# Kernel tuning notes

Hardware: AMD Instinct MI355X
Metric: run time of the kernel (lower is better)

## Reference

```python
import jax, jax.numpy as jnp
import numpy as np
import math

D_MODEL = 1024
N_HEADS = 16
D_HEAD = D_MODEL // N_HEADS
WINDOW = 256
SCALE = 1.0 / math.sqrt(D_HEAD)


def setup_inputs() -> dict:
    key = jax.random.key(0)
    kx, kqkv, kout = jax.random.split(key, 3)
    x = jax.random.normal(kx, (2, 2048, D_MODEL), dtype=jnp.float32)
    # xavier_uniform for nn.Linear weights (shape [out, in] in torch; store as [in, out] for x @ W)
    lim_qkv = math.sqrt(6.0 / (D_MODEL + 3 * D_MODEL))
    W_qkv = jax.random.uniform(kqkv, (D_MODEL, 3 * D_MODEL), dtype=jnp.float32, minval=-lim_qkv, maxval=lim_qkv)
    lim_out = math.sqrt(6.0 / (D_MODEL + D_MODEL))
    W_out = jax.random.uniform(kout, (D_MODEL, D_MODEL), dtype=jnp.float32, minval=-lim_out, maxval=lim_out)
    return {"x": x, "W_qkv": W_qkv, "W_out": W_out}


def _window_mask(seq_len: int) -> jnp.ndarray:
    # causal + sliding window: position i attends to j with i-WINDOW < j <= i
    i = jnp.arange(seq_len)[:, None]
    j = jnp.arange(seq_len)[None, :]
    allowed = (j <= i) & (j > i - WINDOW)
    return jnp.where(allowed, 0.0, -jnp.inf).astype(jnp.float32)


def reference(x, W_qkv, W_out):
    B, S, _ = x.shape
    qkv = x @ W_qkv                                   # [B, S, 3*D]
    qkv = qkv.reshape(B, S, 3, N_HEADS, D_HEAD)
    qkv = jnp.transpose(qkv, (2, 0, 3, 1, 4))         # [3, B, H, S, Dh]
    q, k, v = qkv[0], qkv[1], qkv[2]
    scores = jnp.einsum('bhsd,bhtd->bhst', q, k) * SCALE
    scores = scores + _window_mask(S)[None, None]
    weights = jax.nn.softmax(scores, axis=-1)
    out = jnp.einsum('bhst,bhtd->bhsd', weights, v)   # [B, H, S, Dh]
    out = jnp.transpose(out, (0, 2, 1, 3)).reshape(B, S, D_MODEL)
    return out @ W_out
```

## Files before the change

### kernel.cpp

```cpp
#include <hip/hip_runtime.h>

typedef unsigned short u16;
typedef unsigned int u32;

#define D_MODEL 1024
#define N_HEADS 16
#define D_HEAD 64
#define WIN 256
#define SEQ 2048
#define BATCH 2
#define NROWS (BATCH*SEQ)

typedef short frag_ab __attribute__((ext_vector_type(8)));
typedef float frag_cd __attribute__((ext_vector_type(4)));
typedef float f32x16 __attribute__((ext_vector_type(16)));
typedef u16 u16x8 __attribute__((ext_vector_type(8)));

__device__ __forceinline__ u16 f2bf(float f) {
    union { float f; u32 u; } x; x.f = f;
    u32 r = x.u + 0x7fffu + ((x.u >> 16) & 1u);
    return (u16)(r >> 16);
}

__device__ __forceinline__ void load_lds16(const void* g, void* l) {
    __builtin_amdgcn_global_load_lds(
        (const __attribute__((address_space(1))) void*)g,
        (__attribute__((address_space(3))) void*)l, 16, 0, 0);
}

__device__ __forceinline__ void transpose_tile(const float* __restrict__ W, u16* __restrict__ WT,
                                               int K, int N, int n0, int k0,
                                               int scale_rows, float scale, float (*tile)[33]) {
    int x = threadIdx.x & 31, y = threadIdx.x >> 5;
#pragma unroll
    for (int r = 0; r < 4; r++)
        tile[y + 8 * r][x] = W[(size_t)(k0 + y + 8 * r) * N + n0 + x];
    __syncthreads();
#pragma unroll
    for (int r = 0; r < 4; r++) {
        int nrow = n0 + y + 8 * r;
        float v = tile[x][y + 8 * r];
        if (nrow < scale_rows) v *= scale;
        WT[(size_t)nrow * K + k0 + x] = f2bf(v);
    }
}

__global__ __launch_bounds__(256) void prep_kernel(const float* __restrict__ x,
                                                   const float* __restrict__ W_qkv,
                                                   u16* __restrict__ xb,
                                                   u16* __restrict__ wqkvT,
                                                   float qscale) {
    __shared__ float tile[32][33];
    const int bid = blockIdx.x;
    if (bid < 4096) {
        int idx = bid * 256 + threadIdx.x;
        float4 v = ((const float4*)x)[idx];
        ushort4 o;
        o.x = f2bf(v.x); o.y = f2bf(v.y); o.z = f2bf(v.z); o.w = f2bf(v.w);
        ((ushort4*)xb)[idx] = o;
    } else {
        int t = bid - 4096;
        transpose_tile(W_qkv, wqkvT, D_MODEL, 3 * D_MODEL, (t % 96) * 32, (t / 96) * 32,
                       D_MODEL, qscale, tile);
    }
}

__global__ __launch_bounds__(512, 2) void gemm1_qkv(const u16* __restrict__ A,
                                                    const u16* __restrict__ BT,
                                                    u16* __restrict__ C) {
    constexpr int K = 1024, NLD = 3072, NT = K >> 6;
    __shared__ union SM {
        struct { u16 As[2][256 * 64]; u16 Bs[2][192 * 64]; } s;
        u16 cs[256 * 200];
    } sm;
    const int tid = threadIdx.x;
    const int xcd = blockIdx.x & 7, sblk = blockIdx.x >> 3;
    const int m0 = (sblk & 15) * 256;
    const int n0 = (xcd * 2 + (sblk >> 4)) * 192;
    const int wave = tid >> 6, lane = tid & 63;
    const int wm = (wave >> 1) * 64, wn = (wave & 1) * 96;
    const int l32 = lane & 31, kh = lane >> 5;

    const int r0 = tid >> 3;
    const int w  = (tid & 7) ^ (r0 & 7);
    const u16* aP = A  + (size_t)(m0 + r0) * K + w * 8;
    const u16* bP = BT + (size_t)(n0 + r0) * K + w * 8;

    f32x16 acc[2][3] = {};

#define STAGE(tile_, buf_) do {                                                   \
        const int k0_ = (tile_) * 64;                                             \
        _Pragma("unroll")                                                         \
        for (int u = 0; u < 4; ++u)                                               \
            load_lds16(aP + (size_t)(64 * u) * K + k0_,                           \
                       &sm.s.As[buf_][(tid + 512 * u) * 8]);                      \
        _Pragma("unroll")                                                         \
        for (int u = 0; u < 3; ++u)                                               \
            load_lds16(bP + (size_t)(64 * u) * K + k0_,                           \
                       &sm.s.Bs[buf_][(tid + 512 * u) * 8]);                      \
    } while (0)

    STAGE(0, 0);
    STAGE(1, 1);

    int cur = 0;
    for (int t = 0; t < NT; ++t) {
        if (t + 1 < NT) asm volatile("s_waitcnt vmcnt(7)" ::: "memory");
        else            asm volatile("s_waitcnt vmcnt(0)" ::: "memory");
        asm volatile("s_barrier" ::: "memory");

        const u16* As = sm.s.As[cur];
        const u16* Bs = sm.s.Bs[cur];
#pragma unroll
        for (int ph = 0; ph < 2; ++ph) {
            frag_ab af[2][2], bf[2][3];
#pragma unroll
            for (int kx = 0; kx < 2; ++kx) {
                const int kk = ph * 2 + kx;
                const int csel = ((kk * 2 + kh) ^ (l32 & 7)) * 8;
#pragma unroll
                for (int mt = 0; mt < 2; ++mt)
                    af[kx][mt] = *(const frag_ab*)&As[(wm + mt * 32 + l32) * 64 + csel];
#pragma unroll
                for (int nt = 0; nt < 3; ++nt)
                    bf[kx][nt] = *(const frag_ab*)&Bs[(wn + nt * 32 + l32) * 64 + csel];
            }
            asm volatile("s_barrier" ::: "memory");
            __builtin_amdgcn_s_setprio(1);
#pragma unroll
            for (int kx = 0; kx < 2; ++kx)
#pragma unroll
                for (int mt = 0; mt < 2; ++mt)
#pragma unroll
                    for (int nt = 0; nt < 3; ++nt)
                        acc[mt][nt] = __builtin_amdgcn_mfma_f32_32x32x16_bf16(
                            af[kx][mt], bf[kx][nt], acc[mt][nt], 0, 0, 0);
            __builtin_amdgcn_s_setprio(0);
            asm volatile("s_barrier" ::: "memory");
        }
        if (t + 2 < NT) STAGE(t + 2, cur);
        cur ^= 1;
    }
#undef STAGE

#pragma unroll
    for (int mt = 0; mt < 2; ++mt)
#pragma unroll
        for (int nt = 0; nt < 3; ++nt) {
            const int col = wn + nt * 32 + l32;
#pragma unroll
            for (int reg = 0; reg < 16; ++reg) {
                const int row = wm + mt * 32 + (reg & 3) + 8 * (reg >> 2) + 4 * kh;
                sm.cs[row * 200 + col] = f2bf(acc[mt][nt][reg]);
            }
        }
    asm volatile("s_barrier" ::: "memory");
#pragma unroll
    for (int i = 0; i < 12; ++i) {
        const int idx = tid + 512 * i;
        const int row = idx / 24, c8 = idx % 24;
        u16x8 vv = *(const u16x8*)&sm.cs[row * 200 + c8 * 8];
        *(u16x8*)(C + (size_t)(m0 + row) * NLD + n0 + c8 * 8) = vv;
    }
}

template <bool BF16_OUT, int BM, int MB, int NPER>
__global__ __launch_bounds__(256, 4) void gemm_bk64(const u16* __restrict__ A,
                                                    const u16* __restrict__ BT,
                                                    void* __restrict__ C,
                                                    int M, int N, int K) {
    constexpr int MT = BM / 64;
    __shared__ union SMem {
        struct { u16 As[BM * 64]; u16 Bs[128 * 64]; } s;
        u16 cs[BF16_OUT ? BM * 136 : 1];
    } sm;
    const int tid = threadIdx.x;
    const int xcd = blockIdx.x & 7, sblk = blockIdx.x >> 3;
    const int m0 = (sblk % MB) * BM;
    const int n0 = (xcd * NPER + sblk / MB) * 128;
    const int wave = tid >> 6, lane = tid & 63;
    const int wm = (wave >> 1) * (BM / 2), wn = (wave & 1) * 64;
    const int l32 = lane & 31, kh = lane >> 5;

    f32x16 acc[MT][2] = {};

    const int r0 = tid >> 3;
    const int w  = (tid & 7) ^ (r0 & 7);
    const u16* aP = A  + (size_t)(m0 + r0) * K + w * 8;
    const u16* bP = BT + (size_t)(n0 + r0) * K + w * 8;

    for (int k0 = 0; k0 < K; k0 += 64) {
        __syncthreads();
#pragma unroll
        for (int u = 0; u < BM / 32; u++)
            load_lds16(aP + (size_t)(32 * u) * K + k0, &sm.s.As[(tid + 256 * u) * 8]);
#pragma unroll
        for (int u = 0; u < 4; u++)
            load_lds16(bP + (size_t)(32 * u) * K + k0, &sm.s.Bs[(tid + 256 * u) * 8]);
        __syncthreads();

#pragma unroll
        for (int kk = 0; kk < 4; kk++) {
            const int csel = ((kk * 2 + kh) ^ (l32 & 7)) * 8;
            frag_ab af[MT], bf[2];
#pragma unroll
            for (int t = 0; t < MT; t++)
                af[t] = *(const frag_ab*)&sm.s.As[(wm + t * 32 + l32) * 64 + csel];
#pragma unroll
            for (int t = 0; t < 2; t++)
                bf[t] = *(const frag_ab*)&sm.s.Bs[(wn + t * 32 + l32) * 64 + csel];
#pragma unroll
            for (int mt = 0; mt < MT; mt++)
#pragma unroll
                for (int nt = 0; nt < 2; nt++)
                    acc[mt][nt] = __builtin_amdgcn_mfma_f32_32x32x16_bf16(af[mt], bf[nt], acc[mt][nt], 0, 0, 0);
        }
    }

    if constexpr (BF16_OUT) {
        __syncthreads();
#pragma unroll
        for (int mt = 0; mt < MT; mt++)
#pragma unroll
            for (int nt = 0; nt < 2; nt++) {
                int col = wn + nt * 32 + l32;
#pragma unroll
                for (int reg = 0; reg < 16; reg++) {
                    int row = wm + mt * 32 + (reg & 3) + 8 * (reg >> 2) + 4 * kh;
                    sm.cs[row * 136 + col] = f2bf(acc[mt][nt][reg]);
                }
            }
        __syncthreads();
        const int cc = tid & 15, rb = tid >> 4;
#pragma unroll
        for (int i = 0; i < BM / 16; i++) {
            int row = rb + 16 * i;
            u16x8 vv = *(const u16x8*)&sm.cs[row * 136 + cc * 8];
            *(u16x8*)((u16*)C + (size_t)(m0 + row) * N + n0 + cc * 8) = vv;
        }
    } else {
#pragma unroll
        for (int mt = 0; mt < MT; mt++)
#pragma unroll
            for (int nt = 0; nt < 2; nt++) {
                int col = n0 + wn + nt * 32 + l32;
#pragma unroll
                for (int reg = 0; reg < 16; reg++) {
                    int row = m0 + wm + mt * 32 + (reg & 3) + 8 * (reg >> 2) + 4 * kh;
                    ((float*)C)[(size_t)row * N + col] = acc[mt][nt][reg];
                }
            }
    }
}

__global__ __launch_bounds__(256) void attn_kernel(const u16* __restrict__ qkv, u16* __restrict__ out,
                                                   const float* __restrict__ W_out,
                                                   u16* __restrict__ woutT) {
    __shared__ u16 Ks[2][64 * 64];
    __shared__ u16 Vt[64 * 72];
    __shared__ u16 ps[4][16 * 72];

    if (blockIdx.x >= 1024) {
        int t = blockIdx.x - 1024;
        transpose_tile(W_out, woutT, D_MODEL, D_MODEL, (t & 31) * 32, (t >> 5) * 32,
                       0, 1.0f, (float(*)[33])&Ks[0][0]);
        return;
    }

    const int tid = threadIdx.x;
    const int wave = tid >> 6, lane = tid & 63;
    const int quad = lane >> 4, c16 = lane & 15;

    const int bh = blockIdx.x & 31;
    const int qc = blockIdx.x >> 5;
    const int h  = bh & 15;
    const int b  = bh >> 4;
    const int q0 = qc * 64;
    const int qw0 = q0 + wave * 16;

    frag_ab qf[2];
    {
        const u16* qrow = qkv + (size_t)(b * SEQ + qw0 + c16) * 3072 + h * 64;
        qf[0] = *(const frag_ab*)(qrow + quad * 8);
        qf[1] = *(const frag_ab*)(qrow + 32 + quad * 8);
    }

    float m_r[4], l_r[4];
    frag_cd acc[4] = {};

    const int ntiles = qc < 4 ? qc + 1 : 5;

    const int krow = wave * 16 + (lane >> 3);
    const int kchunk = (lane & 7) ^ (lane >> 3);
    const int vj2 = (tid & 31) * 2, vd8 = tid >> 5;

    const u16* kbase = qkv + (size_t)(b * SEQ + krow) * 3072 + 1024 + h * 64 + kchunk * 8;
    const u16* vbase = qkv + (size_t)(b * SEQ + vj2) * 3072 + 2048 + h * 64 + vd8 * 8;

    u16x8 va, vb;
    {
        const u16* g = kbase + (size_t)q0 * 3072;
        load_lds16(g,            &Ks[0][krow * 64 + (lane & 7) * 8]);
        load_lds16(g + 8 * 3072, &Ks[0][(krow + 8) * 64 + (lane & 7) * 8]);
        const u16* gv = vbase + (size_t)q0 * 3072;
        va = *(const u16x8*)gv;
        vb = *(const u16x8*)(gv + 3072);
#pragma unroll
        for (int dd = 0; dd < 8; dd++)
            *(u32*)&Vt[(vd8 * 8 + dd) * 72 + vj2] = (u32)va[dd] | ((u32)vb[dd] << 16);
    }

    for (int t = 0; t < ntiles; t++) {
        const int cur = t & 1, nxt = cur ^ 1;
        const int j0 = q0 - 64 * t;
        __syncthreads();
        const bool pre = (t + 1 < ntiles);
        if (pre) {
            const u16* g = kbase + (size_t)(j0 - 64) * 3072;
            load_lds16(g,            &Ks[nxt][krow * 64 + (lane & 7) * 8]);
            load_lds16(g + 8 * 3072, &Ks[nxt][(krow + 8) * 64 + (lane & 7) * 8]);
            const u16* gv = vbase + (size_t)(j0 - 64) * 3072;
            va = *(const u16x8*)gv;
            vb = *(const u16x8*)(gv + 3072);
        }

        frag_cd s[4] = {};
#pragma unroll
        for (int kb = 0; kb < 4; kb++) {
            frag_ab kf0 = *(const frag_ab*)&Ks[cur][(kb * 16 + c16) * 64 + ((quad    ) ^ (c16 & 7)) * 8];
            frag_ab kf1 = *(const frag_ab*)&Ks[cur][(kb * 16 + c16) * 64 + ((4 + quad) ^ (c16 & 7)) * 8];
            s[kb] = __builtin_amdgcn_mfma_f32_16x16x32_bf16(qf[0], kf0, s[kb], 0, 0, 0);
            s[kb] = __builtin_amdgcn_mfma_f32_16x16x32_bf16(qf[1], kf1, s[kb], 0, 0, 0);
        }

        if (t == 0) {
#pragma unroll
            for (int reg = 0; reg < 4; reg++) {
                const int i = qw0 + quad * 4 + reg;
#pragma unroll
                for (int kb = 0; kb < 4; kb++)
                    if (q0 + kb * 16 + c16 > i) s[kb][reg] = -1e30f;
            }
        } else if (t == 4) {
#pragma unroll
            for (int reg = 0; reg < 4; reg++) {
                const int i = qw0 + quad * 4 + reg;
#pragma unroll
                for (int kb = 0; kb < 4; kb++)
                    if (j0 + kb * 16 + c16 + WIN <= i) s[kb][reg] = -1e30f;
            }
        }

        float mt_[4];
#pragma unroll
        for (int reg = 0; reg < 4; reg++)
            mt_[reg] = fmaxf(fmaxf(s[0][reg], s[1][reg]), fmaxf(s[2][reg], s[3][reg]));
#pragma unroll
        for (int off = 1; off < 16; off <<= 1)
#pragma unroll
            for (int reg = 0; reg < 4; reg++) mt_[reg] = fmaxf(mt_[reg], __shfl_xor(mt_[reg], off));

        float alpha[4];
        if (t == 0) {
#pragma unroll
            for (int reg = 0; reg < 4; reg++) m_r[reg] = mt_[reg];
        } else {
#pragma unroll
            for (int reg = 0; reg < 4; reg++) {
                float mn = fmaxf(m_r[reg], mt_[reg]);
                alpha[reg] = __builtin_amdgcn_exp2f(m_r[reg] - mn);
                m_r[reg] = mn;
            }
        }

        float rs[4] = {0.f, 0.f, 0.f, 0.f};
#pragma unroll
        for (int kb = 0; kb < 4; kb++)
#pragma unroll
            for (int reg = 0; reg < 4; reg++) {
                float p = __builtin_amdgcn_exp2f(s[kb][reg] - m_r[reg]);
                union { float f; u32 u; } pu; pu.f = p;
                ps[wave][(quad * 4 + reg) * 72 + kb * 16 + c16] = (u16)(pu.u >> 16);
                rs[reg] += p;
            }
#pragma unroll
        for (int off = 1; off < 16; off <<= 1)
#pragma unroll
            for (int reg = 0; reg < 4; reg++) rs[reg] += __shfl_xor(rs[reg], off);

        if (t == 0) {
#pragma unroll
            for (int reg = 0; reg < 4; reg++) l_r[reg] = rs[reg];
        } else {
#pragma unroll
            for (int reg = 0; reg < 4; reg++) l_r[reg] = l_r[reg] * alpha[reg] + rs[reg];
#pragma unroll
            for (int dblk = 0; dblk < 4; dblk++)
#pragma unroll
                for (int reg = 0; reg < 4; reg++) acc[dblk][reg] *= alpha[reg];
        }

#pragma unroll
        for (int js = 0; js < 2; js++) {
            frag_ab pf = *(const frag_ab*)&ps[wave][c16 * 72 + js * 32 + quad * 8];
#pragma unroll
            for (int dblk = 0; dblk < 4; dblk++) {
                frag_ab vf = *(const frag_ab*)&Vt[(dblk * 16 + c16) * 72 + js * 32 + quad * 8];
                acc[dblk] = __builtin_amdgcn_mfma_f32_16x16x32_bf16(pf, vf, acc[dblk], 0, 0, 0);
            }
        }

        if (pre) {
            __syncthreads();
#pragma unroll
            for (int dd = 0; dd < 8; dd++)
                *(u32*)&Vt[(vd8 * 8 + dd) * 72 + vj2] = (u32)va[dd] | ((u32)vb[dd] << 16);
        }
    }

    float inv[4];
#pragma unroll
    for (int reg = 0; reg < 4; reg++) inv[reg] = 1.f / l_r[reg];
#pragma unroll
    for (int dblk = 0; dblk < 4; dblk++)
#pragma unroll
        for (int reg = 0; reg < 4; reg++)
            out[(size_t)(b * SEQ + qw0 + quad * 4 + reg) * 1024 + h * 64 + dblk * 16 + c16] =
                f2bf(acc[dblk][reg] * inv[reg]);
}

extern "C" void kernel_launch(void* const* d_in, const int* in_sizes, int n_in,
                              void* d_out, int out_size, void* d_ws, size_t ws_size,
                              hipStream_t stream) {
    const float* x     = (const float*)d_in[0];
    const float* W_qkv = (const float*)d_in[1];
    const float* W_out = (const float*)d_in[2];
    float* out = (float*)d_out;

    char* ws = (char*)d_ws;
    u16* xb    = (u16*)(ws);
    u16* wqkvT = (u16*)(ws + 8388608);
    u16* woutT = (u16*)(ws + 14680064);
    u16* qkvb  = (u16*)(ws + 16777216);
    u16* attnb = (u16*)(ws + 41943040);

    const float QSCALE = 0.125f * 1.4426950408889634f;

    prep_kernel<<<7168, 256, 0, stream>>>(x, W_qkv, xb, wqkvT, QSCALE);
    gemm1_qkv<<<256, 512, 0, stream>>>(xb, wqkvT, qkvb);
    attn_kernel<<<2048, 256, 0, stream>>>(qkvb, attnb, W_out, woutT);
    gemm_bk64<false, 64, 64, 1><<<512, 256, 0, stream>>>(
        attnb, woutT, out, NROWS, D_MODEL, D_MODEL);
}
```

Measured before the change: 151.6 us.

## Replace output GEMM with double-buffered 128x128 tiled kernel; restructure QKV GEMM phases

Replaces the generic single-buffered output projection GEMM with a dedicated kernel that uses 128x128 tiles, double-buffered LDS staging with async loads, and phased fragment loads with priority hints. It now launches 256 blocks instead of 512, each doing more work. The QKV GEMM inner loop is also changed from two phases of two k-steps to four single k-step phases, which adds more barriers but keeps fewer fragments live. The intent is to overlap global loads with MFMA in the output GEMM and reduce per-tile overhead, at the cost of fewer blocks to fill the CUs.

```diff
diff --git a/kernel.cpp b/kernel.cpp
--- a/kernel.cpp
+++ b/kernel.cpp
@@ -112,29 +112,23 @@
         const u16* As = sm.s.As[cur];
         const u16* Bs = sm.s.Bs[cur];
 #pragma unroll
-        for (int ph = 0; ph < 2; ++ph) {
-            frag_ab af[2][2], bf[2][3];
-#pragma unroll
-            for (int kx = 0; kx < 2; ++kx) {
-                const int kk = ph * 2 + kx;
-                const int csel = ((kk * 2 + kh) ^ (l32 & 7)) * 8;
-#pragma unroll
-                for (int mt = 0; mt < 2; ++mt)
-                    af[kx][mt] = *(const frag_ab*)&As[(wm + mt * 32 + l32) * 64 + csel];
-#pragma unroll
-                for (int nt = 0; nt < 3; ++nt)
-                    bf[kx][nt] = *(const frag_ab*)&Bs[(wn + nt * 32 + l32) * 64 + csel];
-            }
+        for (int kk = 0; kk < 4; ++kk) {
+            const int csel = ((kk * 2 + kh) ^ (l32 & 7)) * 8;
+            frag_ab af[2], bf[3];
+#pragma unroll
+            for (int mt = 0; mt < 2; ++mt)
+                af[mt] = *(const frag_ab*)&As[(wm + mt * 32 + l32) * 64 + csel];
+#pragma unroll
+            for (int nt = 0; nt < 3; ++nt)
+                bf[nt] = *(const frag_ab*)&Bs[(wn + nt * 32 + l32) * 64 + csel];
             asm volatile("s_barrier" ::: "memory");
             __builtin_amdgcn_s_setprio(1);
 #pragma unroll
-            for (int kx = 0; kx < 2; ++kx)
-#pragma unroll
-                for (int mt = 0; mt < 2; ++mt)
-#pragma unroll
-                    for (int nt = 0; nt < 3; ++nt)
-                        acc[mt][nt] = __builtin_amdgcn_mfma_f32_32x32x16_bf16(
-                            af[kx][mt], bf[kx][nt], acc[mt][nt], 0, 0, 0);
+            for (int mt = 0; mt < 2; ++mt)
+#pragma unroll
+                for (int nt = 0; nt < 3; ++nt)
+                    acc[mt][nt] = __builtin_amdgcn_mfma_f32_32x32x16_bf16(
+                        af[mt], bf[nt], acc[mt][nt], 0, 0, 0);
             __builtin_amdgcn_s_setprio(0);
             asm volatile("s_barrier" ::: "memory");
         }
@@ -164,93 +158,92 @@
     }
 }
 
-template <bool BF16_OUT, int BM, int MB, int NPER>
-__global__ __launch_bounds__(256, 4) void gemm_bk64(const u16* __restrict__ A,
-                                                    const u16* __restrict__ BT,
-                                                    void* __restrict__ C,
-                                                    int M, int N, int K) {
-    constexpr int MT = BM / 64;
-    __shared__ union SMem {
-        struct { u16 As[BM * 64]; u16 Bs[128 * 64]; } s;
-        u16 cs[BF16_OUT ? BM * 136 : 1];
-    } sm;
+__global__ __launch_bounds__(256) void gemm2_out(const u16* __restrict__ A,
+                                                 const u16* __restrict__ BT,
+                                                 float* __restrict__ C) {
+    constexpr int K = 1024, N = 1024, NT = K >> 6;
+    __shared__ struct { u16 As[2][128 * 64]; u16 Bs[2][128 * 64]; } sm;
     const int tid = threadIdx.x;
     const int xcd = blockIdx.x & 7, sblk = blockIdx.x >> 3;
-    const int m0 = (sblk % MB) * BM;
-    const int n0 = (xcd * NPER + sblk / MB) * 128;
+    const int m0 = sblk * 128;
+    const int n0 = xcd * 128;
     const int wave = tid >> 6, lane = tid & 63;
-    const int wm = (wave >> 1) * (BM / 2), wn = (wave & 1) * 64;
+    const int wm = (wave >> 1) * 64, wn = (wave & 1) * 64;
     const int l32 = lane & 31, kh = lane >> 5;
-
-    f32x16 acc[MT][2] = {};
 
     const int r0 = tid >> 3;
     const int w  = (tid & 7) ^ (r0 & 7);
     const u16* aP = A  + (size_t)(m0 + r0) * K + w * 8;
     const u16* bP = BT + (size_t)(n0 + r0) * K + w * 8;
 
-    for (int k0 = 0; k0 < K; k0 += 64) {
-        __syncthreads();
-#pragma unroll
-        for (int u = 0; u < BM / 32; u++)
-            load_lds16(aP + (size_t)(32 * u) * K + k0, &sm.s.As[(tid + 256 * u) * 8]);
-#pragma unroll
-        for (int u = 0; u < 4; u++)
-            load_lds16(bP + (size_t)(32 * u) * K + k0, &sm.s.Bs[(tid + 256 * u) * 8]);
-        __syncthreads();
-
-#pragma unroll
-        for (int kk = 0; kk < 4; kk++) {
-            const int csel = ((kk * 2 + kh) ^ (l32 & 7)) * 8;
-            frag_ab af[MT], bf[2];
-#pragma unroll
-            for (int t = 0; t < MT; t++)
-                af[t] = *(const frag_ab*)&sm.s.As[(wm + t * 32 + l32) * 64 + csel];
-#pragma unroll
-            for (int t = 0; t < 2; t++)
-                bf[t] = *(const frag_ab*)&sm.s.Bs[(wn + t * 32 + l32) * 64 + csel];
-#pragma unroll
-            for (int mt = 0; mt < MT; mt++)
-#pragma unroll
-                for (int nt = 0; nt < 2; nt++)
-                    acc[mt][nt] = __builtin_amdgcn_mfma_f32_32x32x16_bf16(af[mt], bf[nt], acc[mt][nt], 0, 0, 0);
-        }
-    }
-
-    if constexpr (BF16_OUT) {
-        __syncthreads();
-#pragma unroll
-        for (int mt = 0; mt < MT; mt++)
-#pragma unroll
-            for (int nt = 0; nt < 2; nt++) {
-                int col = wn + nt * 32 + l32;
-#pragma unroll
-                for (int reg = 0; reg < 16; reg++) {
-                    int row = wm + mt * 32 + (reg & 3) + 8 * (reg >> 2) + 4 * kh;
-                    sm.cs[row * 136 + col] = f2bf(acc[mt][nt][reg]);
-                }
-            }
-        __syncthreads();
-        const int cc = tid & 15, rb = tid >> 4;
-#pragma unroll
-        for (int i = 0; i < BM / 16; i++) {
-            int row = rb + 16 * i;
-            u16x8 vv = *(const u16x8*)&sm.cs[row * 136 + cc * 8];
-            *(u16x8*)((u16*)C + (size_t)(m0 + row) * N + n0 + cc * 8) = vv;
-        }
-    } else {
-#pragma unroll
-        for (int mt = 0; mt < MT; mt++)
-#pragma unroll
-            for (int nt = 0; nt < 2; nt++) {
-                int col = n0 + wn + nt * 32 + l32;
-#pragma unroll
-                for (int reg = 0; reg < 16; reg++) {
-                    int row = m0 + wm + mt * 32 + (reg & 3) + 8 * (reg >> 2) + 4 * kh;
-                    ((float*)C)[(size_t)row * N + col] = acc[mt][nt][reg];
-                }
-            }
-    }
+    f32x16 acc[2][2] = {};
+
+#define STAGE2(tile_, buf_) do {                                                  \
+        const int k0_ = (tile_) * 64;                                             \
+        _Pragma("unroll")                                                         \
+        for (int u = 0; u < 4; ++u)                                               \
+            load_lds16(aP + (size_t)(32 * u) * K + k0_,                           \
+                       &sm.As[buf_][(tid + 256 * u) * 8]);                        \
+        _Pragma("unroll")                                                         \
+        for (int u = 0; u < 4; ++u)                                               \
+            load_lds16(bP + (size_t)(32 * u) * K + k0_,                           \
+                       &sm.Bs[buf_][(tid + 256 * u) * 8]);                        \
+    } while (0)
+
+    STAGE2(0, 0);
+    STAGE2(1, 1);
+
+    int cur = 0;
+    for (int t = 0; t < NT; ++t) {
+        if (t + 1 < NT) asm volatile("s_waitcnt vmcnt(8)" ::: "memory");
+        else            asm volatile("s_waitcnt vmcnt(0)" ::: "memory");
+        asm volatile("s_barrier" ::: "memory");
+
+        const u16* As = sm.As[cur];
+        const u16* Bs = sm.Bs[cur];
+#pragma unroll
+        for (int ph = 0; ph < 2; ++ph) {
+            frag_ab af[2][2], bf[2][2];
+#pragma unroll
+            for (int kx = 0; kx < 2; ++kx) {
+                const int kk = ph * 2 + kx;
+                const int csel = ((kk * 2 + kh) ^ (l32 & 7)) * 8;
+#pragma unroll
+                for (int mt = 0; mt < 2; ++mt)
+                    af[kx][mt] = *(const frag_ab*)&As[(wm + mt * 32 + l32) * 64 + csel];
+#pragma unroll
+                for (int nt = 0; nt < 2; ++nt)
+                    bf[kx][nt] = *(const frag_ab*)&Bs[(wn + nt * 32 + l32) * 64 + csel];
+            }
+            asm volatile("s_barrier" ::: "memory");
+            __builtin_amdgcn_s_setprio(1);
+#pragma unroll
+            for (int kx = 0; kx < 2; ++kx)
+#pragma unroll
+                for (int mt = 0; mt < 2; ++mt)
+#pragma unroll
+                    for (int nt = 0; nt < 2; ++nt)
+                        acc[mt][nt] = __builtin_amdgcn_mfma_f32_32x32x16_bf16(
+                            af[kx][mt], bf[kx][nt], acc[mt][nt], 0, 0, 0);
+            __builtin_amdgcn_s_setprio(0);
+            asm volatile("s_barrier" ::: "memory");
+        }
+        if (t + 2 < NT) STAGE2(t + 2, cur);
+        cur ^= 1;
+    }
+#undef STAGE2
+
+#pragma unroll
+    for (int mt = 0; mt < 2; ++mt)
+#pragma unroll
+        for (int nt = 0; nt < 2; ++nt) {
+            const int col = n0 + wn + nt * 32 + l32;
+#pragma unroll
+            for (int reg = 0; reg < 16; ++reg) {
+                const int row = m0 + wm + mt * 32 + (reg & 3) + 8 * (reg >> 2) + 4 * kh;
+                C[(size_t)row * N + col] = acc[mt][nt][reg];
+            }
+        }
 }
 
 __global__ __launch_bounds__(256) void attn_kernel(const u16* __restrict__ qkv, u16* __restrict__ out,
@@ -449,6 +442,5 @@
     prep_kernel<<<7168, 256, 0, stream>>>(x, W_qkv, xb, wqkvT, QSCALE);
     gemm1_qkv<<<256, 512, 0, stream>>>(xb, wqkvT, qkvb);
     attn_kernel<<<2048, 256, 0, stream>>>(qkvb, attnb, W_out, woutT);
-    gemm_bk64<false, 64, 64, 1><<<512, 256, 0, stream>>>(
-        attnb, woutT, out, NROWS, D_MODEL, D_MODEL);
-}
+    gemm2_out<<<256, 256, 0, stream>>>(attnb, woutT, out);
+}
```

Measured after the change: 149.8 us. Within noise of the previous version (-1.2%).
